# Kernel optimization log

Measured on AMD Instinct MI355X. Metric: run time of the kernel, lower is better.

## Reference

```python
import jax, jax.numpy as jnp
import numpy as np

DIM_IN, DIM_Q, DIM_K = 768, 64, 64
B, S = 8, 2048

def setup_inputs() -> dict:
    key = jax.random.key(0)
    ks = jax.random.split(key, 9)
    lim_q = 1.0 / np.sqrt(DIM_IN)
    return {
        'query': jax.random.normal(ks[0], (B, S, DIM_IN), jnp.float32),
        'key':   jax.random.normal(ks[1], (B, S, DIM_IN), jnp.float32),
        'value': jax.random.normal(ks[2], (B, S, DIM_IN), jnp.float32),
        'Wq': jax.random.uniform(ks[3], (DIM_IN, DIM_Q), jnp.float32, -lim_q, lim_q),
        'bq': jax.random.uniform(ks[4], (DIM_Q,), jnp.float32, -lim_q, lim_q),
        'Wk': jax.random.uniform(ks[5], (DIM_IN, DIM_K), jnp.float32, -lim_q, lim_q),
        'bk': jax.random.uniform(ks[6], (DIM_K,), jnp.float32, -lim_q, lim_q),
        'Wv': jax.random.uniform(ks[7], (DIM_IN, DIM_K), jnp.float32, -lim_q, lim_q),
        'bv': jax.random.uniform(ks[8], (DIM_K,), jnp.float32, -lim_q, lim_q),
    }

def reference(query, key, value, Wq, bq, Wk, bk, Wv, bv):
    # linear projections: [B,S,dim_in] -> [B,S,64]
    q = jnp.einsum('bsd,dq->bsq', query, Wq) + bq
    k = jnp.einsum('bsd,dk->bsk', key, Wk) + bk
    v = jnp.einsum('bsd,dk->bsk', value, Wv) + bv
    # cosine attention: L2-normalize q and k along feature dim
    qn = q / jnp.linalg.norm(q, axis=-1, keepdims=True)
    kn = k / jnp.linalg.norm(k, axis=-1, keepdims=True)
    scale = jnp.sqrt(jnp.asarray(q.shape[-1], q.dtype))  # scaled=True
    scores = jnp.einsum('bqk,bsk->bqs', qn, kn) / scale  # [B,S,S]
    attn = jax.nn.softmax(scores, axis=-1)
    return jnp.einsum('bqs,bsk->bqk', attn, v)  # [B,S,64]
```

## Files before the change

kernel.cpp:

```cpp
#include <hip/hip_runtime.h>
#include <hip/hip_bf16.h>

#define DIN 768
#define DD  64
#define NB  8
#define SS  2048
#define NROWS (NB*SS)

typedef __bf16 bf16;
typedef __attribute__((ext_vector_type(8))) __bf16 bf16x8;
typedef __attribute__((ext_vector_type(4))) __bf16 bf16x4;
typedef __attribute__((ext_vector_type(4))) float f32x4;

#define MFMA16 __builtin_amdgcn_mfma_f32_16x16x32_bf16


__global__ __launch_bounds__(256) void k_wt(const float* __restrict__ Wq,
                                            const float* __restrict__ Wk,
                                            const float* __restrict__ Wv,
                                            bf16* __restrict__ wt)
{
    int t = blockIdx.y;
    const float* W = (t == 0) ? Wq : ((t == 1) ? Wk : Wv);
    bf16* o = wt + (size_t)t * DD * DIN;
    int k0 = blockIdx.x * 64;

    __shared__ float tile[64][65];

    #pragma unroll
    for (int i = 0; i < 4; ++i) {
        int idx = threadIdx.x + i * 256;
        int row = idx >> 4;
        int c4  = (idx & 15) * 4;
        f32x4 u = *(const f32x4*)(W + (size_t)(k0 + row) * DD + c4);
        tile[c4 + 0][row] = u[0]; tile[c4 + 1][row] = u[1];
        tile[c4 + 2][row] = u[2]; tile[c4 + 3][row] = u[3];
    }
    __syncthreads();
    #pragma unroll
    for (int i = 0; i < 4; ++i) {
        int idx = threadIdx.x + i * 256;
        int col = idx >> 4;
        int k4  = (idx & 15) * 4;
        bf16x4 u;
        u[0] = (bf16)tile[col][k4 + 0]; u[1] = (bf16)tile[col][k4 + 1];
        u[2] = (bf16)tile[col][k4 + 2]; u[3] = (bf16)tile[col][k4 + 3];
        *(bf16x4*)(o + (size_t)col * DIN + k0 + k4) = u;
    }
}

__global__ __launch_bounds__(256) void k_proj(
    const float* __restrict__ Xq, const float* __restrict__ Xk, const float* __restrict__ Xv,
    const float* __restrict__ bq, const float* __restrict__ bk, const float* __restrict__ bv,
    const bf16* __restrict__ wt,
    bf16* __restrict__ qn, bf16* __restrict__ kn, bf16* __restrict__ vT)
{
    int t = blockIdx.y;
    const float* X    = (t == 0) ? Xq : ((t == 1) ? Xk : Xv);
    const float* bias = (t == 0) ? bq : ((t == 1) ? bk : bv);
    const bf16*  w    = wt + (size_t)t * DD * DIN;

    int row0 = blockIdx.x * 64;
    int lane = threadIdx.x & 63;
    int wid  = threadIdx.x >> 6;
    int lr = lane & 15, lk = lane >> 4;
    int r  = row0 + wid * 16 + lr;

    const float* xp = X + (size_t)r * DIN + lk * 8;
    const bf16*  wp = w + (size_t)lr * DIN + lk * 8;

    f32x4 acc[4] = {};

    f32x4  px0[3], px1[3];
    bf16x8 pw[3][4];
    #pragma unroll
    for (int p = 0; p < 3; ++p) {
        int kk = p * 32;
        px0[p] = *(const f32x4*)(xp + kk);
        px1[p] = *(const f32x4*)(xp + kk + 4);
        #pragma unroll
        for (int cf = 0; cf < 4; ++cf)
            pw[p][cf] = *(const bf16x8*)(wp + (size_t)cf * 16 * DIN + kk);
    }

    #pragma unroll
    for (int it = 0; it < 24; ++it) {
        const int slot = it % 3;
        bf16x8 a;
        a[0] = (bf16)px0[slot][0]; a[1] = (bf16)px0[slot][1];
        a[2] = (bf16)px0[slot][2]; a[3] = (bf16)px0[slot][3];
        a[4] = (bf16)px1[slot][0]; a[5] = (bf16)px1[slot][1];
        a[6] = (bf16)px1[slot][2]; a[7] = (bf16)px1[slot][3];
        bf16x8 w0 = pw[slot][0], w1 = pw[slot][1], w2 = pw[slot][2], w3 = pw[slot][3];
        if (it + 3 < 24) {
            int kk = (it + 3) * 32;
            px0[slot] = *(const f32x4*)(xp + kk);
            px1[slot] = *(const f32x4*)(xp + kk + 4);
            #pragma unroll
            for (int cf = 0; cf < 4; ++cf)
                pw[slot][cf] = *(const bf16x8*)(wp + (size_t)cf * 16 * DIN + kk);
        }
        acc[0] = MFMA16(a, w0, acc[0], 0, 0, 0);
        acc[1] = MFMA16(a, w1, acc[1], 0, 0, 0);
        acc[2] = MFMA16(a, w2, acc[2], 0, 0, 0);
        acc[3] = MFMA16(a, w3, acc[3], 0, 0, 0);
    }

    #pragma unroll
    for (int cf = 0; cf < 4; ++cf) {
        float bc = bias[cf * 16 + lr];
        acc[cf][0] += bc; acc[cf][1] += bc; acc[cf][2] += bc; acc[cf][3] += bc;
    }

    if (t < 2) {
        const float c = (t == 0) ? 0.18033688011112042f  : 1.0f;
        f32x4 ss = {};
        #pragma unroll
        for (int cf = 0; cf < 4; ++cf)
            #pragma unroll
            for (int reg = 0; reg < 4; ++reg)
                ss[reg] += acc[cf][reg] * acc[cf][reg];
        #pragma unroll
        for (int reg = 0; reg < 4; ++reg) {
            float v = ss[reg];
            v += __shfl_xor(v, 1); v += __shfl_xor(v, 2);
            v += __shfl_xor(v, 4); v += __shfl_xor(v, 8);
            ss[reg] = v;
        }
        bf16* o = (t == 0) ? qn : kn;
        #pragma unroll
        for (int reg = 0; reg < 4; ++reg) {
            float sc = __builtin_amdgcn_rsqf(ss[reg]) * c;
            int rr = row0 + wid * 16 + lk * 4 + reg;
            #pragma unroll
            for (int cf = 0; cf < 4; ++cf)
                o[(size_t)rr * DD + cf * 16 + lr] = (bf16)(acc[cf][reg] * sc);
        }
    } else {
        __shared__ bf16 vt[64][72];
        #pragma unroll
        for (int reg = 0; reg < 4; ++reg)
            #pragma unroll
            for (int cf = 0; cf < 4; ++cf)
                vt[cf * 16 + lr][wid * 16 + lk * 4 + reg] = (bf16)acc[cf][reg];
        __syncthreads();
        int bb = row0 >> 11, s0 = row0 & (SS - 1);
        #pragma unroll
        for (int j = 0; j < 4; ++j) {
            int f4 = threadIdx.x + j * 256;
            int dv = f4 >> 4, s4 = f4 & 15;
            bf16x4 u;
            u[0] = vt[dv][s4 * 4 + 0]; u[1] = vt[dv][s4 * 4 + 1];
            u[2] = vt[dv][s4 * 4 + 2]; u[3] = vt[dv][s4 * 4 + 3];
            *(bf16x4*)(vT + ((size_t)(bb * DD + dv)) * SS + s0 + s4 * 4) = u;
        }
    }
}

__global__ __launch_bounds__(256) void k_attn(
    const bf16* __restrict__ qn, const bf16* __restrict__ kn,
    const bf16* __restrict__ vT, float* __restrict__ out)
{
    int b  = blockIdx.y;
    int q0 = blockIdx.x * 16;
    int lane = threadIdx.x & 63, wid = threadIdx.x >> 6;
    int lr = lane & 15, lk = lane >> 4;

    __shared__ float num_all[4][16][68];
    __shared__ float den_lds[4][16];
    bf16* p_lds = (bf16*)&num_all[wid][0][0];
    float (*num_lds)[68] = num_all[wid];

    const bf16* qb = qn + ((size_t)(b * SS + q0 + lr)) * DD + lk * 8;
    bf16x8 qf0 = *(const bf16x8*)(qb);
    bf16x8 qf1 = *(const bf16x8*)(qb + 32);

    const bf16* kb = kn + (size_t)b * SS * DD;
    const bf16* vb = vT + (size_t)b * DD * SS;

    f32x4 oacc[4] = {};
    f32x4 den     = {};

    int sbeg = wid * (SS / 4);
    for (int s = sbeg; s < sbeg + SS / 4; s += 64) {
        f32x4 sacc[4] = {};
        #pragma unroll
        for (int cf = 0; cf < 4; ++cf) {
            const bf16* kp = kb + (size_t)(s + cf * 16 + lr) * DD + lk * 8;
            bf16x8 k0 = *(const bf16x8*)(kp);
            bf16x8 k1 = *(const bf16x8*)(kp + 32);
            sacc[cf] = MFMA16(qf0, k0, sacc[cf], 0, 0, 0);
            sacc[cf] = MFMA16(qf1, k1, sacc[cf], 0, 0, 0);
        }
        #pragma unroll
        for (int reg = 0; reg < 4; ++reg) {
            int prow = lk * 4 + reg;
            int swz  = (prow & 7) << 4;
            #pragma unroll
            for (int cf = 0; cf < 4; ++cf) {
                float p = __builtin_amdgcn_exp2f(sacc[cf][reg]);
                den[reg] += p;
                *(bf16*)((char*)p_lds + prow * 128 + ((((cf * 16 + lr) * 2)) ^ swz)) = (bf16)p;
            }
        }
        __builtin_amdgcn_sched_barrier(0);
        bf16x8 pf0, pf1;
        {
            int swz = (lr & 7) << 4;
            pf0 = *(const bf16x8*)((char*)p_lds + lr * 128 + (((lk * 8) * 2) ^ swz));
            pf1 = *(const bf16x8*)((char*)p_lds + lr * 128 + (((32 + lk * 8) * 2) ^ swz));
        }
        #pragma unroll
        for (int cf = 0; cf < 4; ++cf) {
            const bf16* vp = vb + (size_t)(cf * 16 + lr) * SS + s + lk * 8;
            bf16x8 v0 = *(const bf16x8*)(vp);
            bf16x8 v1 = *(const bf16x8*)(vp + 32);
            oacc[cf] = MFMA16(pf0, v0, oacc[cf], 0, 0, 0);
            oacc[cf] = MFMA16(pf1, v1, oacc[cf], 0, 0, 0);
        }
    }

    #pragma unroll
    for (int reg = 0; reg < 4; ++reg) {
        float d = den[reg];
        d += __shfl_xor(d, 1); d += __shfl_xor(d, 2);
        d += __shfl_xor(d, 4); d += __shfl_xor(d, 8);
        if (lr == 0) den_lds[wid][lk * 4 + reg] = d;
        #pragma unroll
        for (int cf = 0; cf < 4; ++cf)
            num_lds[lk * 4 + reg][cf * 16 + lr] = oacc[cf][reg];
    }
    __syncthreads();

    float* ob = out + ((size_t)b * SS + q0) * DD;
    #pragma unroll
    for (int j = 0; j < 4; ++j) {
        int e = threadIdx.x + j * 256;
        int q = e >> 6, dv = e & 63;
        float n = num_all[0][q][dv] + num_all[1][q][dv] + num_all[2][q][dv] + num_all[3][q][dv];
        float d = den_lds[0][q] + den_lds[1][q] + den_lds[2][q] + den_lds[3][q];
        ob[e] = n / d;
    }
}

extern "C" void kernel_launch(void* const* d_in, const int* in_sizes, int n_in,
                              void* d_out, int out_size, void* d_ws, size_t ws_size,
                              hipStream_t stream) {
    const float* Xq = (const float*)d_in[0];
    const float* Xk = (const float*)d_in[1];
    const float* Xv = (const float*)d_in[2];
    const float* Wq = (const float*)d_in[3];
    const float* bq = (const float*)d_in[4];
    const float* Wk = (const float*)d_in[5];
    const float* bk = (const float*)d_in[6];
    const float* Wv = (const float*)d_in[7];
    const float* bv = (const float*)d_in[8];

    bf16* ws = (bf16*)d_ws;
    bf16* wt = ws;
    bf16* qn = ws + 3 * DD * DIN;
    bf16* kn = qn + (size_t)NROWS * DD;
    bf16* vT = kn + (size_t)NROWS * DD;
    float* o = (float*)d_out;

    hipLaunchKernelGGL(k_wt,   dim3(12, 3),  dim3(256), 0, stream, Wq, Wk, Wv, wt);
    hipLaunchKernelGGL(k_proj, dim3(256, 3), dim3(256), 0, stream,
                       Xq, Xk, Xv, bq, bk, bv, wt, qn, kn, vT);
    hipLaunchKernelGGL(k_attn, dim3(128, 8), dim3(256), 0, stream, qn, kn, vT, o);
}
```

Measured before the change: 250.5 us.

## Stream projection X tiles via direct global-to-LDS loads with swizzled FIFO

The projection kernel now stages the fp32 input rows through a per-wave 4-slot LDS ring filled by global_load_lds DMA. Reads use an XOR swizzle to avoid bank conflicts, and an explicit vmcnt wait keeps three steps in flight. Weights drop from triple-buffered registers to a single next-step prefetch. This aims to cut register pressure and make the input loads coalesced, at the cost of extra LDS traffic and hand-tuned wait counts.

```diff
diff --git a/kernel.cpp b/kernel.cpp
--- a/kernel.cpp
+++ b/kernel.cpp
@@ -64,47 +64,62 @@
     int lane = threadIdx.x & 63;
     int wid  = threadIdx.x >> 6;
     int lr = lane & 15, lk = lane >> 4;
-    int r  = row0 + wid * 16 + lr;
-
-    const float* xp = X + (size_t)r * DIN + lk * 8;
-    const bf16*  wp = w + (size_t)lr * DIN + lk * 8;
+    int rw = row0 + wid * 16;
+
+    __shared__ float xfifo[4][4][16 * 32];
+    float* slab = &xfifo[wid][0][0];
+
+    const float* s0 = X + (size_t)(rw + (lane >> 3)) * DIN + (((lane & 7) ^ (lane >> 3)) << 2);
+    const float* s1 = s0 + 8 * DIN;
+
+#define XDMA(step) do {                                                              \
+    float* ld_ = slab + ((step) % 4) * 512;                                          \
+    __builtin_amdgcn_global_load_lds(                                                \
+        (const __attribute__((address_space(1))) unsigned int*)(s0 + (step) * 32),   \
+        (__attribute__((address_space(3))) unsigned int*)ld_, 16, 0, 0);             \
+    __builtin_amdgcn_global_load_lds(                                                \
+        (const __attribute__((address_space(1))) unsigned int*)(s1 + (step) * 32),   \
+        (__attribute__((address_space(3))) unsigned int*)(ld_ + 256), 16, 0, 0);     \
+} while (0)
+
+    const bf16* wp = w + (size_t)lr * DIN + lk * 8;
+
+    XDMA(0); XDMA(1); XDMA(2);
+    bf16x8 wc0 = *(const bf16x8*)(wp + 0 * 16 * DIN);
+    bf16x8 wc1 = *(const bf16x8*)(wp + 1 * 16 * DIN);
+    bf16x8 wc2 = *(const bf16x8*)(wp + 2 * 16 * DIN);
+    bf16x8 wc3 = *(const bf16x8*)(wp + 3 * 16 * DIN);
 
     f32x4 acc[4] = {};
-
-    f32x4  px0[3], px1[3];
-    bf16x8 pw[3][4];
-    #pragma unroll
-    for (int p = 0; p < 3; ++p) {
-        int kk = p * 32;
-        px0[p] = *(const f32x4*)(xp + kk);
-        px1[p] = *(const f32x4*)(xp + kk + 4);
-        #pragma unroll
-        for (int cf = 0; cf < 4; ++cf)
-            pw[p][cf] = *(const bf16x8*)(wp + (size_t)cf * 16 * DIN + kk);
-    }
+    const int xsw = (lr & 7) * 4;
 
     #pragma unroll
     for (int it = 0; it < 24; ++it) {
-        const int slot = it % 3;
+        asm volatile("s_waitcnt vmcnt(8)" ::: "memory");
+        __builtin_amdgcn_sched_barrier(0);
+
+        const float* sl = slab + (it % 4) * 512;
+        f32x4 xa = *(const f32x4*)(sl + lr * 32 + ((lk * 8)     ^ xsw));
+        f32x4 xb = *(const f32x4*)(sl + lr * 32 + ((lk * 8 + 4) ^ xsw));
+
+        if (it + 3 < 24) XDMA(it + 3);
+        const int tn = (it + 1 < 24) ? it + 1 : 23;
+        bf16x8 wn0 = *(const bf16x8*)(wp + 0 * 16 * DIN + tn * 32);
+        bf16x8 wn1 = *(const bf16x8*)(wp + 1 * 16 * DIN + tn * 32);
+        bf16x8 wn2 = *(const bf16x8*)(wp + 2 * 16 * DIN + tn * 32);
+        bf16x8 wn3 = *(const bf16x8*)(wp + 3 * 16 * DIN + tn * 32);
+
         bf16x8 a;
-        a[0] = (bf16)px0[slot][0]; a[1] = (bf16)px0[slot][1];
-        a[2] = (bf16)px0[slot][2]; a[3] = (bf16)px0[slot][3];
-        a[4] = (bf16)px1[slot][0]; a[5] = (bf16)px1[slot][1];
-        a[6] = (bf16)px1[slot][2]; a[7] = (bf16)px1[slot][3];
-        bf16x8 w0 = pw[slot][0], w1 = pw[slot][1], w2 = pw[slot][2], w3 = pw[slot][3];
-        if (it + 3 < 24) {
-            int kk = (it + 3) * 32;
-            px0[slot] = *(const f32x4*)(xp + kk);
-            px1[slot] = *(const f32x4*)(xp + kk + 4);
-            #pragma unroll
-            for (int cf = 0; cf < 4; ++cf)
-                pw[slot][cf] = *(const bf16x8*)(wp + (size_t)cf * 16 * DIN + kk);
-        }
-        acc[0] = MFMA16(a, w0, acc[0], 0, 0, 0);
-        acc[1] = MFMA16(a, w1, acc[1], 0, 0, 0);
-        acc[2] = MFMA16(a, w2, acc[2], 0, 0, 0);
-        acc[3] = MFMA16(a, w3, acc[3], 0, 0, 0);
-    }
+        a[0] = (bf16)xa[0]; a[1] = (bf16)xa[1]; a[2] = (bf16)xa[2]; a[3] = (bf16)xa[3];
+        a[4] = (bf16)xb[0]; a[5] = (bf16)xb[1]; a[6] = (bf16)xb[2]; a[7] = (bf16)xb[3];
+
+        acc[0] = MFMA16(a, wc0, acc[0], 0, 0, 0);
+        acc[1] = MFMA16(a, wc1, acc[1], 0, 0, 0);
+        acc[2] = MFMA16(a, wc2, acc[2], 0, 0, 0);
+        acc[3] = MFMA16(a, wc3, acc[3], 0, 0, 0);
+        wc0 = wn0; wc1 = wn1; wc2 = wn2; wc3 = wn3;
+    }
+#undef XDMA
 
     #pragma unroll
     for (int cf = 0; cf < 4; ++cf) {
@@ -144,7 +159,7 @@
             for (int cf = 0; cf < 4; ++cf)
                 vt[cf * 16 + lr][wid * 16 + lk * 4 + reg] = (bf16)acc[cf][reg];
         __syncthreads();
-        int bb = row0 >> 11, s0 = row0 & (SS - 1);
+        int bb = row0 >> 11, s0v = row0 & (SS - 1);
         #pragma unroll
         for (int j = 0; j < 4; ++j) {
             int f4 = threadIdx.x + j * 256;
@@ -152,7 +167,7 @@
             bf16x4 u;
             u[0] = vt[dv][s4 * 4 + 0]; u[1] = vt[dv][s4 * 4 + 1];
             u[2] = vt[dv][s4 * 4 + 2]; u[3] = vt[dv][s4 * 4 + 3];
-            *(bf16x4*)(vT + ((size_t)(bb * DD + dv)) * SS + s0 + s4 * 4) = u;
+            *(bf16x4*)(vT + ((size_t)(bb * DD + dv)) * SS + s0v + s4 * 4) = u;
         }
     }
 }
```

Result: slower. 258.1 us (+3.0%).

## Split projection K dimension across waves with LDS reduction and smaller row tiles

Applied to the files above, without the earlier changes.

The projection kernel now gives each block 16 rows instead of 64, and each of its four waves handles a quarter of the 768-wide reduction. Partial sums are combined through shared memory before the bias, normalization and stores. The grid grows fourfold (3072 blocks), which should fill the GPU better and expose more memory parallelism, and a launch-bounds occupancy hint is added. In exchange it drops the explicit register prefetch pipeline, adds an LDS reduction and extra barriers, and rereads the weights once per block.

```diff
diff --git a/kernel.cpp b/kernel.cpp
--- a/kernel.cpp
+++ b/kernel.cpp
@@ -49,7 +49,7 @@
     }
 }
 
-__global__ __launch_bounds__(256) void k_proj(
+__global__ __launch_bounds__(256, 4) void k_proj(
     const float* __restrict__ Xq, const float* __restrict__ Xk, const float* __restrict__ Xv,
     const float* __restrict__ bq, const float* __restrict__ bk, const float* __restrict__ bv,
     const bf16* __restrict__ wt,
@@ -60,100 +60,69 @@
     const float* bias = (t == 0) ? bq : ((t == 1) ? bk : bv);
     const bf16*  w    = wt + (size_t)t * DD * DIN;
 
-    int row0 = blockIdx.x * 64;
+    int row0 = blockIdx.x * 16;
     int lane = threadIdx.x & 63;
     int wid  = threadIdx.x >> 6;
     int lr = lane & 15, lk = lane >> 4;
-    int r  = row0 + wid * 16 + lr;
-
-    const float* xp = X + (size_t)r * DIN + lk * 8;
-    const bf16*  wp = w + (size_t)lr * DIN + lk * 8;
+
+    const float* xp = X + (size_t)(row0 + lr) * DIN + wid * 192 + lk * 8;
+    const bf16*  wp = w + (size_t)lr * DIN + wid * 192 + lk * 8;
 
     f32x4 acc[4] = {};
-
-    f32x4  px0[3], px1[3];
-    bf16x8 pw[3][4];
-    #pragma unroll
-    for (int p = 0; p < 3; ++p) {
-        int kk = p * 32;
-        px0[p] = *(const f32x4*)(xp + kk);
-        px1[p] = *(const f32x4*)(xp + kk + 4);
+    #pragma unroll
+    for (int it = 0; it < 6; ++it) {
+        int kk = it * 32;
+        f32x4 x0 = *(const f32x4*)(xp + kk);
+        f32x4 x1 = *(const f32x4*)(xp + kk + 4);
+        bf16x8 a;
+        a[0] = (bf16)x0[0]; a[1] = (bf16)x0[1]; a[2] = (bf16)x0[2]; a[3] = (bf16)x0[3];
+        a[4] = (bf16)x1[0]; a[5] = (bf16)x1[1]; a[6] = (bf16)x1[2]; a[7] = (bf16)x1[3];
+        #pragma unroll
+        for (int cf = 0; cf < 4; ++cf) {
+            bf16x8 bfr = *(const bf16x8*)(wp + (size_t)cf * 16 * DIN + kk);
+            acc[cf] = MFMA16(a, bfr, acc[cf], 0, 0, 0);
+        }
+    }
+
+    __shared__ float red[4][16][68];
+    __shared__ bf16  vts[64][18];
+    #pragma unroll
+    for (int reg = 0; reg < 4; ++reg)
         #pragma unroll
         for (int cf = 0; cf < 4; ++cf)
-            pw[p][cf] = *(const bf16x8*)(wp + (size_t)cf * 16 * DIN + kk);
-    }
-
-    #pragma unroll
-    for (int it = 0; it < 24; ++it) {
-        const int slot = it % 3;
-        bf16x8 a;
-        a[0] = (bf16)px0[slot][0]; a[1] = (bf16)px0[slot][1];
-        a[2] = (bf16)px0[slot][2]; a[3] = (bf16)px0[slot][3];
-        a[4] = (bf16)px1[slot][0]; a[5] = (bf16)px1[slot][1];
-        a[6] = (bf16)px1[slot][2]; a[7] = (bf16)px1[slot][3];
-        bf16x8 w0 = pw[slot][0], w1 = pw[slot][1], w2 = pw[slot][2], w3 = pw[slot][3];
-        if (it + 3 < 24) {
-            int kk = (it + 3) * 32;
-            px0[slot] = *(const f32x4*)(xp + kk);
-            px1[slot] = *(const f32x4*)(xp + kk + 4);
-            #pragma unroll
-            for (int cf = 0; cf < 4; ++cf)
-                pw[slot][cf] = *(const bf16x8*)(wp + (size_t)cf * 16 * DIN + kk);
-        }
-        acc[0] = MFMA16(a, w0, acc[0], 0, 0, 0);
-        acc[1] = MFMA16(a, w1, acc[1], 0, 0, 0);
-        acc[2] = MFMA16(a, w2, acc[2], 0, 0, 0);
-        acc[3] = MFMA16(a, w3, acc[3], 0, 0, 0);
-    }
-
-    #pragma unroll
-    for (int cf = 0; cf < 4; ++cf) {
-        float bc = bias[cf * 16 + lr];
-        acc[cf][0] += bc; acc[cf][1] += bc; acc[cf][2] += bc; acc[cf][3] += bc;
-    }
+            red[wid][lk * 4 + reg][cf * 16 + lr] = acc[cf][reg];
+    __syncthreads();
+
+    int row = threadIdx.x >> 4, seg = threadIdx.x & 15;
+    float val[4];
+    #pragma unroll
+    for (int j = 0; j < 4; ++j)
+        val[j] = red[0][row][seg * 4 + j] + red[1][row][seg * 4 + j]
+               + red[2][row][seg * 4 + j] + red[3][row][seg * 4 + j]
+               + bias[seg * 4 + j];
 
     if (t < 2) {
+        float ss = val[0]*val[0] + val[1]*val[1] + val[2]*val[2] + val[3]*val[3];
+        ss += __shfl_xor(ss, 1); ss += __shfl_xor(ss, 2);
+        ss += __shfl_xor(ss, 4); ss += __shfl_xor(ss, 8);
         const float c = (t == 0) ? 0.18033688011112042f  : 1.0f;
-        f32x4 ss = {};
-        #pragma unroll
-        for (int cf = 0; cf < 4; ++cf)
-            #pragma unroll
-            for (int reg = 0; reg < 4; ++reg)
-                ss[reg] += acc[cf][reg] * acc[cf][reg];
-        #pragma unroll
-        for (int reg = 0; reg < 4; ++reg) {
-            float v = ss[reg];
-            v += __shfl_xor(v, 1); v += __shfl_xor(v, 2);
-            v += __shfl_xor(v, 4); v += __shfl_xor(v, 8);
-            ss[reg] = v;
-        }
+        float sc = __builtin_amdgcn_rsqf(ss) * c;
         bf16* o = (t == 0) ? qn : kn;
-        #pragma unroll
-        for (int reg = 0; reg < 4; ++reg) {
-            float sc = __builtin_amdgcn_rsqf(ss[reg]) * c;
-            int rr = row0 + wid * 16 + lk * 4 + reg;
-            #pragma unroll
-            for (int cf = 0; cf < 4; ++cf)
-                o[(size_t)rr * DD + cf * 16 + lr] = (bf16)(acc[cf][reg] * sc);
-        }
+        bf16x4 u;
+        u[0] = (bf16)(val[0] * sc); u[1] = (bf16)(val[1] * sc);
+        u[2] = (bf16)(val[2] * sc); u[3] = (bf16)(val[3] * sc);
+        *(bf16x4*)(o + (size_t)(row0 + row) * DD + seg * 4) = u;
     } else {
-        __shared__ bf16 vt[64][72];
-        #pragma unroll
-        for (int reg = 0; reg < 4; ++reg)
-            #pragma unroll
-            for (int cf = 0; cf < 4; ++cf)
-                vt[cf * 16 + lr][wid * 16 + lk * 4 + reg] = (bf16)acc[cf][reg];
+        #pragma unroll
+        for (int j = 0; j < 4; ++j)
+            vts[seg * 4 + j][row] = (bf16)val[j];
         __syncthreads();
         int bb = row0 >> 11, s0 = row0 & (SS - 1);
-        #pragma unroll
-        for (int j = 0; j < 4; ++j) {
-            int f4 = threadIdx.x + j * 256;
-            int dv = f4 >> 4, s4 = f4 & 15;
-            bf16x4 u;
-            u[0] = vt[dv][s4 * 4 + 0]; u[1] = vt[dv][s4 * 4 + 1];
-            u[2] = vt[dv][s4 * 4 + 2]; u[3] = vt[dv][s4 * 4 + 3];
-            *(bf16x4*)(vT + ((size_t)(bb * DD + dv)) * SS + s0 + s4 * 4) = u;
-        }
+        int dv = threadIdx.x >> 2, c4 = threadIdx.x & 3;
+        bf16x4 u;
+        u[0] = vts[dv][c4 * 4 + 0]; u[1] = vts[dv][c4 * 4 + 1];
+        u[2] = vts[dv][c4 * 4 + 2]; u[3] = vts[dv][c4 * 4 + 3];
+        *(bf16x4*)(vT + ((size_t)(bb * DD + dv)) * SS + s0 + c4 * 4) = u;
     }
 }
 
@@ -263,8 +232,8 @@
     bf16* vT = kn + (size_t)NROWS * DD;
     float* o = (float*)d_out;
 
-    hipLaunchKernelGGL(k_wt,   dim3(12, 3),  dim3(256), 0, stream, Wq, Wk, Wv, wt);
-    hipLaunchKernelGGL(k_proj, dim3(256, 3), dim3(256), 0, stream,
+    hipLaunchKernelGGL(k_wt,   dim3(12, 3),   dim3(256), 0, stream, Wq, Wk, Wv, wt);
+    hipLaunchKernelGGL(k_proj, dim3(1024, 3), dim3(256), 0, stream,
                        Xq, Xk, Xv, bq, bk, bv, wt, qn, kn, vT);
-    hipLaunchKernelGGL(k_attn, dim3(128, 8), dim3(256), 0, stream, qn, kn, vT, o);
-}
+    hipLaunchKernelGGL(k_attn, dim3(128, 8),  dim3(256), 0, stream, qn, kn, vT, o);
+}
```

After: 264.3 us. 5.5% more time.
